# Optimization experiments

Hardware: AMD Instinct MI355X
Metric: run time of the kernel (lower is better)

## Reference

```python
import jax, jax.numpy as jnp
import numpy as np
import math

EMBED = 512
DIM2 = 768

def setup_inputs() -> dict:
    key = jax.random.key(0)
    ks = jax.random.split(key, 14)
    B, L1, L2 = 16, 2048, 1024
    s1 = 1.0 / math.sqrt(EMBED)
    s2 = 1.0 / math.sqrt(DIM2)
    inp = {
        'input_tensor1': jax.random.normal(ks[0], (B, EMBED, L1), jnp.float32),
        'input_tensor2': jax.random.normal(ks[1], (B, DIM2, L2), jnp.float32),
        # Linear params for modality 1 (512 -> 512)
        'Wq1': jax.random.normal(ks[2], (EMBED, EMBED), jnp.float32) * s1,
        'bq1': jnp.zeros((EMBED,), jnp.float32),
        'Wk1': jax.random.normal(ks[3], (EMBED, EMBED), jnp.float32) * s1,
        'bk1': jnp.zeros((EMBED,), jnp.float32),
        'Wv1': jax.random.normal(ks[4], (EMBED, EMBED), jnp.float32) * s1,
        'bv1': jnp.zeros((EMBED,), jnp.float32),
        # Linear params for modality 2 (768 -> 512)
        'Wq2': jax.random.normal(ks[5], (DIM2, EMBED), jnp.float32) * s2,
        'bq2': jnp.zeros((EMBED,), jnp.float32),
        'Wk2': jax.random.normal(ks[6], (DIM2, EMBED), jnp.float32) * s2,
        'bk2': jnp.zeros((EMBED,), jnp.float32),
        'Wv2': jax.random.normal(ks[7], (DIM2, EMBED), jnp.float32) * s2,
        'bv2': jnp.zeros((EMBED,), jnp.float32),
    }
    return inp


def reference(input_tensor1, input_tensor2,
              Wq1, bq1, Wk1, bk1, Wv1, bv1,
              Wq2, bq2, Wk2, bk2, Wv2, bv2):
    scale = 1.0 / math.sqrt(EMBED)
    # [B, C, L] -> [B, L, C]
    x1 = jnp.swapaxes(input_tensor1, 1, 2)  # [B, L1, 512]
    x2 = jnp.swapaxes(input_tensor2, 1, 2)  # [B, L2, 768]
    q1 = x1 @ Wq1 + bq1  # [B, L1, E]
    k1 = x1 @ Wk1 + bk1
    v1 = x1 @ Wv1 + bv1
    q2 = x2 @ Wq2 + bq2  # [B, L2, E]
    k2 = x2 @ Wk2 + bk2
    v2 = x2 @ Wv2 + bv2
    # direction 1: queries from modality 2 attend to modality 1
    scores1 = jnp.einsum('bif,bjf->bij', q2, k1) * scale  # [B, L2, L1]
    probs1 = jax.nn.sigmoid(scores1)
    ctx1 = jnp.einsum('bij,bjf->bif', probs1, v1)  # [B, L2, E]
    # direction 2: queries from modality 1 attend to modality 2
    scores2 = jnp.einsum('bif,bjf->bij', q1, k2) * scale  # [B, L1, L2]
    probs2 = jax.nn.sigmoid(scores2)
    ctx2 = jnp.einsum('bij,bjf->bif', probs2, v2)  # [B, L1, E]
    return (ctx2, probs2, ctx1, probs1)
```

## Files before the change

kernel.cpp:

```cpp
#include <hip/hip_runtime.h>
#include <hip/hip_bf16.h>

#define DEVFN __device__ __forceinline__

typedef __attribute__((ext_vector_type(4))) float f32x4;
typedef __attribute__((ext_vector_type(8))) short s16x8;
typedef __attribute__((ext_vector_type(2))) short s16x2;
typedef __attribute__((ext_vector_type(8))) __bf16 bf16x8;

union FragU { s16x8 s; bf16x8 b; };

DEVFN short f2bs(float x) {
  union { __hip_bfloat16 h; short s; } u;
  u.h = __float2bfloat16(x);
  return u.s;
}

DEVFN void gload16(const void* g, void* l) {
  __builtin_amdgcn_global_load_lds(
      (const __attribute__((address_space(1))) void*)g,
      (__attribute__((address_space(3))) void*)l, 16, 0, 0);
}

__global__ __launch_bounds__(256) void transpose_cvt(
    const float* __restrict__ in, short* __restrict__ out, int C, int L) {
  __shared__ float tile[64][33];
  const int l0 = blockIdx.x * 32, c0 = blockIdx.y * 64;
  const size_t base = (size_t)blockIdx.z * C * L;
  const int tx = threadIdx.x, ty = threadIdx.y;
#pragma unroll
  for (int i = ty; i < 64; i += 8)
    tile[i][tx] = in[base + (size_t)(c0 + i) * L + l0 + tx];
  __syncthreads();
#pragma unroll
  for (int i = ty; i < 32; i += 8) {
    s16x2 v;
    v[0] = f2bs(tile[2 * tx][i]);
    v[1] = f2bs(tile[2 * tx + 1][i]);
    *(s16x2*)&out[base + (size_t)(l0 + i) * C + c0 + 2 * tx] = v;
  }
}

__global__ __launch_bounds__(256) void prep_weights(
    const float* __restrict__ Wq1, const float* __restrict__ Wk1,
    const float* __restrict__ Wv1, const float* __restrict__ Wq2,
    const float* __restrict__ Wk2, const float* __restrict__ Wv2,
    short* wq1t, short* wk1t, short* wv1t,
    short* wq2t, short* wk2t, short* wv2t,
    const float* __restrict__ bq1, const float* __restrict__ bk1,
    const float* __restrict__ bq2, const float* __restrict__ bk2,
    float* b1c, float* b2c) {
  const int z = blockIdx.z;
  if (z == 6) {
    if (blockIdx.y != 0 || blockIdx.x >= 8) return;
    const int bx = blockIdx.x;
    const int tid = threadIdx.y * 32 + threadIdx.x;
    const int i = (bx & 3) * 256 + tid;
    const float* s = (bx < 4) ? ((i < 512) ? bq1 : bk1)
                              : ((i < 512) ? bq2 : bk2);
    float* d = (bx < 4) ? b1c : b2c;
    d[i] = s[i & 511];
    return;
  }
  const float* W; short* O; int C;
  switch (z) {
    case 0: W = Wq1; O = wq1t; C = 512; break;
    case 1: W = Wk1; O = wk1t; C = 512; break;
    case 2: W = Wv1; O = wv1t; C = 512; break;
    case 3: W = Wq2; O = wq2t; C = 768; break;
    case 4: W = Wk2; O = wk2t; C = 768; break;
    default: W = Wv2; O = wv2t; C = 768; break;
  }
  if (blockIdx.y * 64 >= (unsigned)C) return;
  const int L = 512;
  __shared__ float tile[64][33];
  const int l0 = blockIdx.x * 32, c0 = blockIdx.y * 64;
  const int tx = threadIdx.x, ty = threadIdx.y;
#pragma unroll
  for (int i = ty; i < 64; i += 8)
    tile[i][tx] = W[(size_t)(c0 + i) * L + l0 + tx];
  __syncthreads();
#pragma unroll
  for (int i = ty; i < 32; i += 8) {
    s16x2 v;
    v[0] = f2bs(tile[2 * tx][i]);
    v[1] = f2bs(tile[2 * tx + 1][i]);
    *(s16x2*)&O[(size_t)(l0 + i) * C + c0 + 2 * tx] = v;
  }
}

template <int OUTMODE, int BIASMODE>
__global__ __launch_bounds__(512, 2) void gemm8(
    const short* __restrict__ Ap, const short* __restrict__ Btp,
    const float* __restrict__ bias, void* __restrict__ Cptr,
    short* __restrict__ C2p,
    int K, int lda, int ldb, int ldc,
    long long sA, long long sB, long long sC, float scale) {
  __shared__ __align__(16) char smem[4 * 32768];
  const int tid = threadIdx.x;
  const int lane = tid & 63, wid = tid >> 6;
  const int wm = wid >> 2, wn = wid & 3;
  const int zb = blockIdx.z;
  const int m0 = blockIdx.y * 256, n0 = blockIdx.x * 256;
  const char* Ab = (const char*)(Ap + (size_t)zb * sA);
  const char* Bb = (const char*)(Btp + (size_t)zb * sB);
  const size_t lda2 = (size_t)lda * 2, ldb2 = (size_t)ldb * 2;

  int s_r[2], s_cb[2];
#pragma unroll
  for (int i = 0; i < 2; ++i) {
    const int d = i * 8192 + tid * 16;
    const int line = d >> 7, half = (d >> 6) & 1, q = d & 63;
    s_r[i] = line * 2 + half;
    s_cb[i] = q ^ ((line & 3) << 4);
  }

  f32x4 acc[8][4] = {};
  const int frow = lane & 15, fkg = lane >> 4;

  int ra[8], rb[4];
#pragma unroll
  for (int mf = 0; mf < 8; ++mf) {
    const int R = wm * 128 + mf * 16 + frow;
    ra[mf] = (R >> 1) * 128 + (R & 1) * 64 + ((fkg * 16) ^ (((R >> 1) & 3) << 4));
  }
#pragma unroll
  for (int nf = 0; nf < 4; ++nf) {
    const int R = wn * 64 + nf * 16 + frow;
    rb[nf] = (R >> 1) * 128 + (R & 1) * 64 + ((fkg * 16) ^ (((R >> 1) & 3) << 4));
  }

  const int NT = K >> 5;

#define STAGE8(t)                                                        \
  {                                                                      \
    char* base_ = smem + ((t) & 3) * 32768;                              \
    const size_t kb_ = (size_t)(t) * 64;                                 \
    _Pragma("unroll")                                                    \
    for (int i = 0; i < 2; ++i) {                                        \
      gload16(Ab + (size_t)(m0 + s_r[i]) * lda2 + kb_ + s_cb[i],         \
              base_ + i * 8192 + tid * 16);                              \
      gload16(Bb + (size_t)(n0 + s_r[i]) * ldb2 + kb_ + s_cb[i],         \
              base_ + 16384 + i * 8192 + tid * 16);                      \
    }                                                                    \
  }

  STAGE8(0);
  if (NT > 1) STAGE8(1);
  if (NT > 2) STAGE8(2);
  if (NT > 2)      asm volatile("s_waitcnt vmcnt(8)" ::: "memory");
  else if (NT > 1) asm volatile("s_waitcnt vmcnt(4)" ::: "memory");
  else             asm volatile("s_waitcnt vmcnt(0)" ::: "memory");
  __builtin_amdgcn_sched_barrier(0);
  __builtin_amdgcn_s_barrier();
  __builtin_amdgcn_sched_barrier(0);

  for (int t = 0; t < NT; ++t) {
    if (t + 3 < NT) STAGE8(t + 3);
    const char* la = smem + (t & 3) * 32768;
    const char* lb = la + 16384;
    FragU fa[8], fb[4];
#pragma unroll
    for (int mf = 0; mf < 8; ++mf) fa[mf].s = *(const s16x8*)(la + ra[mf]);
#pragma unroll
    for (int nf = 0; nf < 4; ++nf) fb[nf].s = *(const s16x8*)(lb + rb[nf]);
    __builtin_amdgcn_s_setprio(1);
#pragma unroll
    for (int mf = 0; mf < 8; ++mf)
#pragma unroll
      for (int nf = 0; nf < 4; ++nf)
        acc[mf][nf] = __builtin_amdgcn_mfma_f32_16x16x32_bf16(
            fa[mf].b, fb[nf].b, acc[mf][nf], 0, 0, 0);
    __builtin_amdgcn_s_setprio(0);
    if (t + 3 < NT) {
      asm volatile("s_waitcnt vmcnt(8)" ::: "memory");
    } else if (t + 2 < NT) {
      asm volatile("s_waitcnt vmcnt(4)" ::: "memory");
    } else if (t + 1 < NT) {
      asm volatile("s_waitcnt vmcnt(0)" ::: "memory");
    } else {
      break;
    }
    __builtin_amdgcn_sched_barrier(0);
    __builtin_amdgcn_s_barrier();
    __builtin_amdgcn_sched_barrier(0);
  }
#undef STAGE8

  const int rbase = (lane >> 4) * 4, cbase = lane & 15;
#pragma unroll
  for (int mf = 0; mf < 8; ++mf) {
#pragma unroll
    for (int nf = 0; nf < 4; ++nf) {
      const int gcol = n0 + wn * 64 + nf * 16 + cbase;
      float bn = (BIASMODE == 1) ? bias[gcol] : 0.f;
#pragma unroll
      for (int r = 0; r < 4; ++r) {
        const int grow = m0 + wm * 128 + mf * 16 + rbase + r;
        const size_t idx = (size_t)zb * sC + (size_t)grow * ldc + gcol;
        float v = acc[mf][nf][r];
        if constexpr (BIASMODE == 2) v += bias[grow]; else v += bn;
        if constexpr (OUTMODE == 0) {
          ((short*)Cptr)[idx] = f2bs(v);
        } else if constexpr (OUTMODE == 1) {
          ((float*)Cptr)[idx] = v;
        } else if constexpr (OUTMODE == 2) {
          ((float*)Cptr)[idx] = 1.0f / (1.0f + __expf(-v * scale));
        } else {
          float p = 1.0f / (1.0f + __expf(-v * scale));
          ((float*)Cptr)[idx] = p;
          C2p[idx] = f2bs(p);
        }
      }
    }
  }
}

template <int OUTMODE, int BIASMODE, int AF32>
__global__ __launch_bounds__(256) void gemm_bt(
    const void* __restrict__ Aptr, const short* __restrict__ Btp,
    const float* __restrict__ bias, void* __restrict__ Cptr,
    short* __restrict__ C2p,
    int K, int lda, int ldb, int ldc,
    long long sA, long long sB, long long sC, float scale) {
  __shared__ __align__(16) short lsA[128 * 64];
  __shared__ __align__(16) short lsB[128 * 64];
  const int tid = threadIdx.x;
  const int lane = tid & 63, wid = tid >> 6;
  const int zb = blockIdx.z;
  const int m0 = blockIdx.y * 128, n0 = blockIdx.x * 128;
  const short* Ab = AF32 ? nullptr : (const short*)Aptr + (size_t)zb * sA;
  const float* Af = AF32 ? (const float*)Aptr + (size_t)zb * sA : nullptr;
  const short* Bt = Btp + (size_t)zb * sB;

  f32x4 acc[4][4] = {};
  const int woffM = (wid >> 1) * 64, woffN = (wid & 1) * 64;
  const int frow = lane & 15, fkg = lane >> 4;

  for (int k0 = 0; k0 < K; k0 += 64) {
    if (k0) __syncthreads();
    if constexpr (!AF32) {
#pragma unroll
      for (int i = 0; i < 4; ++i) {
        const int f = i * 4096 + tid * 16;
        const int row = f >> 7, colb = f & 127;
        gload16((const char*)Ab + ((size_t)(m0 + row) * lda + k0) * 2 + colb,
                (char*)lsA + f);
      }
    } else {
#pragma unroll
      for (int i = 0; i < 8; ++i) {
        int f = tid + i * 256;
        int row = f >> 4, c4 = f & 15;
        f32x4 v = *(const f32x4*)&Af[(size_t)(m0 + row) * lda + k0 + c4 * 4];
        union { short s[4]; unsigned long long q; } cv;
#pragma unroll
        for (int j = 0; j < 4; ++j) cv.s[j] = f2bs(v[j]);
        *(unsigned long long*)&lsA[row * 64 + c4 * 4] = cv.q;
      }
    }
#pragma unroll
    for (int i = 0; i < 4; ++i) {
      const int f = i * 4096 + tid * 16;
      const int row = f >> 7, colb = f & 127;
      gload16((const char*)Bt + ((size_t)(n0 + row) * ldb + k0) * 2 + colb,
              (char*)lsB + f);
    }
    __syncthreads();
#pragma unroll
    for (int kk = 0; kk < 2; ++kk) {
      const int kb = kk * 32 + fkg * 8;
      FragU fa[4], fb[4];
#pragma unroll
      for (int mf = 0; mf < 4; ++mf)
        fa[mf].s = *(const s16x8*)&lsA[(woffM + mf * 16 + frow) * 64 + kb];
#pragma unroll
      for (int nf = 0; nf < 4; ++nf)
        fb[nf].s = *(const s16x8*)&lsB[(woffN + nf * 16 + frow) * 64 + kb];
#pragma unroll
      for (int mf = 0; mf < 4; ++mf)
#pragma unroll
        for (int nf = 0; nf < 4; ++nf)
          acc[mf][nf] = __builtin_amdgcn_mfma_f32_16x16x32_bf16(
              fa[mf].b, fb[nf].b, acc[mf][nf], 0, 0, 0);
    }
  }

  const int rbase = (lane >> 4) * 4, cbase = lane & 15;
#pragma unroll
  for (int mf = 0; mf < 4; ++mf) {
#pragma unroll
    for (int nf = 0; nf < 4; ++nf) {
      const int gcol = n0 + woffN + nf * 16 + cbase;
      float bn = (BIASMODE == 1) ? bias[gcol] : 0.f;
#pragma unroll
      for (int r = 0; r < 4; ++r) {
        const int grow = m0 + woffM + mf * 16 + rbase + r;
        const size_t idx = (size_t)zb * sC + (size_t)grow * ldc + gcol;
        float v = acc[mf][nf][r];
        if constexpr (BIASMODE == 2) v += bias[grow]; else v += bn;
        if constexpr (OUTMODE == 0) {
          ((short*)Cptr)[idx] = f2bs(v);
        } else if constexpr (OUTMODE == 1) {
          ((float*)Cptr)[idx] = v;
        } else if constexpr (OUTMODE == 2) {
          ((float*)Cptr)[idx] = 1.0f / (1.0f + __expf(-v * scale));
        } else {
          float p = 1.0f / (1.0f + __expf(-v * scale));
          ((float*)Cptr)[idx] = p;
          C2p[idx] = f2bs(p);
        }
      }
    }
  }
}

extern "C" void kernel_launch(void* const* d_in, const int* in_sizes, int n_in,
                              void* d_out, int out_size, void* d_ws, size_t ws_size,
                              hipStream_t stream) {
  const float* in1 = (const float*)d_in[0];
  const float* in2 = (const float*)d_in[1];
  const float* Wq1 = (const float*)d_in[2];  const float* bq1 = (const float*)d_in[3];
  const float* Wk1 = (const float*)d_in[4];  const float* bk1 = (const float*)d_in[5];
  const float* Wv1 = (const float*)d_in[6];  const float* bv1 = (const float*)d_in[7];
  const float* Wq2 = (const float*)d_in[8];  const float* bq2 = (const float*)d_in[9];
  const float* Wk2 = (const float*)d_in[10]; const float* bk2 = (const float*)d_in[11];
  const float* Wv2 = (const float*)d_in[12]; const float* bv2 = (const float*)d_in[13];

  float* out = (float*)d_out;
  float* ctx2   = out;
  float* probs2 = out + (size_t)16 * 2048 * 512;
  float* ctx1   = probs2 + (size_t)16 * 2048 * 1024;
  float* probs1 = ctx1 + (size_t)16 * 1024 * 512;

  char* ws = (char*)d_ws;
  constexpr size_t O_WQ1T = 0;
  constexpr size_t O_WK1T = O_WQ1T + (size_t)512 * 512 * 2;
  constexpr size_t O_WV1T = O_WK1T + (size_t)512 * 512 * 2;
  constexpr size_t O_WQ2T = O_WV1T + (size_t)512 * 512 * 2;
  constexpr size_t O_WK2T = O_WQ2T + (size_t)768 * 512 * 2;
  constexpr size_t O_WV2T = O_WK2T + (size_t)768 * 512 * 2;
  constexpr size_t O_B1   = O_WV2T + (size_t)768 * 512 * 2;
  constexpr size_t O_B2   = O_B1 + 4096;
  constexpr size_t O_QK1  = O_B2 + 4096;
  constexpr size_t O_V1T  = O_QK1 + (size_t)32768 * 1024 * 2;
  constexpr size_t O_QK2  = O_V1T + (size_t)16 * 512 * 2048 * 2;
  constexpr size_t O_V2T  = O_QK2 + (size_t)16384 * 1024 * 2;
  constexpr size_t O_X1B  = O_V2T + (size_t)16 * 512 * 1024 * 2;
  constexpr size_t O_X2B  = O_X1B + (size_t)32768 * 512 * 2;
  constexpr size_t O_PB1  = O_X2B + (size_t)16384 * 768 * 2;
  constexpr size_t O_PB2  = O_PB1 + (size_t)16 * 1024 * 2048 * 2;
  constexpr size_t NEED_A = O_PB2 + (size_t)16 * 2048 * 1024 * 2;
  constexpr size_t NEED_B = O_PB1;

  short* wq1t = (short*)(ws + O_WQ1T);
  short* wk1t = (short*)(ws + O_WK1T);
  short* wv1t = (short*)(ws + O_WV1T);
  short* wq2t = (short*)(ws + O_WQ2T);
  short* wk2t = (short*)(ws + O_WK2T);
  short* wv2t = (short*)(ws + O_WV2T);
  float* b1c  = (float*)(ws + O_B1);
  float* b2c  = (float*)(ws + O_B2);
  short* qk1  = (short*)(ws + O_QK1);
  short* v1t  = (short*)(ws + O_V1T);
  short* qk2  = (short*)(ws + O_QK2);
  short* v2t  = (short*)(ws + O_V2T);
  short* x1b  = (short*)(ws + O_X1B);
  short* x2b  = (short*)(ws + O_X2B);
  short* pb1  = (short*)(ws + O_PB1);
  short* pb2  = (short*)(ws + O_PB2);

  const bool tierA = ws_size >= NEED_A;
  const bool tierB = ws_size >= NEED_B;
  if (!tierB) { x1b = (short*)probs1; x2b = (short*)probs2; }

  dim3 blk256(256), blk512(512);
  dim3 blkT(32, 8);

  transpose_cvt<<<dim3(64, 8, 16), blkT, 0, stream>>>(in1, x1b, 512, 2048);
  transpose_cvt<<<dim3(32, 12, 16), blkT, 0, stream>>>(in2, x2b, 768, 1024);
  prep_weights<<<dim3(16, 12, 7), blkT, 0, stream>>>(
      Wq1, Wk1, Wv1, Wq2, Wk2, Wv2, wq1t, wk1t, wv1t, wq2t, wk2t, wv2t,
      bq1, bk1, bq2, bk2, b1c, b2c);

  const float scale = 0.04419417382415922f;
  const short* q1p = qk1;
  const short* k1p = qk1 + 512;
  const short* q2p = qk2;
  const short* k2p = qk2 + 512;

  if (tierA) {
    gemm8<0, 1><<<dim3(4, 128, 1), blk512, 0, stream>>>(
        x1b, wq1t, b1c, qk1, nullptr, 512, 512, 512, 1024, 0, 0, 0, 1.f);
    gemm8<0, 1><<<dim3(4, 64, 1), blk512, 0, stream>>>(
        x2b, wq2t, b2c, qk2, nullptr, 768, 768, 768, 1024, 0, 0, 0, 1.f);
    gemm8<0, 2><<<dim3(8, 2, 16), blk512, 0, stream>>>(
        wv1t, x1b, bv1, v1t, nullptr, 512, 512, 512, 2048,
        0, (long long)2048 * 512, (long long)512 * 2048, 1.f);
    gemm8<0, 2><<<dim3(4, 2, 16), blk512, 0, stream>>>(
        wv2t, x2b, bv2, v2t, nullptr, 768, 768, 768, 1024,
        0, (long long)1024 * 768, (long long)512 * 1024, 1.f);
    gemm8<3, 0><<<dim3(8, 4, 16), blk512, 0, stream>>>(
        q2p, k1p, nullptr, probs1, pb1, 512, 1024, 1024, 2048,
        (long long)1024 * 1024, (long long)2048 * 1024, (long long)1024 * 2048, scale);
    gemm8<3, 0><<<dim3(4, 8, 16), blk512, 0, stream>>>(
        q1p, k2p, nullptr, probs2, pb2, 512, 1024, 1024, 1024,
        (long long)2048 * 1024, (long long)1024 * 1024, (long long)2048 * 1024, scale);
    gemm8<1, 0><<<dim3(2, 4, 16), blk512, 0, stream>>>(
        pb1, v1t, nullptr, ctx1, nullptr, 2048, 2048, 2048, 512,
        (long long)1024 * 2048, (long long)512 * 2048, (long long)1024 * 512, 1.f);
    gemm8<1, 0><<<dim3(2, 8, 16), blk512, 0, stream>>>(
        pb2, v2t, nullptr, ctx2, nullptr, 1024, 1024, 1024, 512,
        (long long)2048 * 1024, (long long)512 * 1024, (long long)2048 * 512, 1.f);
  } else {
    gemm_bt<0, 1, 0><<<dim3(8, 256, 1), blk256, 0, stream>>>(
        x1b, wq1t, b1c, qk1, nullptr, 512, 512, 512, 1024, 0, 0, 0, 1.f);
    gemm_bt<0, 1, 0><<<dim3(8, 128, 1), blk256, 0, stream>>>(
        x2b, wq2t, b2c, qk2, nullptr, 768, 768, 768, 1024, 0, 0, 0, 1.f);
    gemm_bt<0, 2, 0><<<dim3(16, 4, 16), blk256, 0, stream>>>(
        wv1t, x1b, bv1, v1t, nullptr, 512, 512, 512, 2048,
        0, (long long)2048 * 512, (long long)512 * 2048, 1.f);
    gemm_bt<0, 2, 0><<<dim3(8, 4, 16), blk256, 0, stream>>>(
        wv2t, x2b, bv2, v2t, nullptr, 768, 768, 768, 1024,
        0, (long long)1024 * 768, (long long)512 * 1024, 1.f);
    gemm_bt<2, 0, 0><<<dim3(16, 8, 16), blk256, 0, stream>>>(
        q2p, k1p, nullptr, probs1, nullptr, 512, 1024, 1024, 2048,
        (long long)1024 * 1024, (long long)2048 * 1024, (long long)1024 * 2048, scale);
    gemm_bt<2, 0, 0><<<dim3(8, 16, 16), blk256, 0, stream>>>(
        q1p, k2p, nullptr, probs2, nullptr, 512, 1024, 1024, 1024,
        (long long)2048 * 1024, (long long)1024 * 1024, (long long)2048 * 1024, scale);
    gemm_bt<1, 0, 1><<<dim3(4, 8, 16), blk256, 0, stream>>>(
        probs1, v1t, nullptr, ctx1, nullptr, 2048, 2048, 2048, 512,
        (long long)1024 * 2048, (long long)512 * 2048, (long long)1024 * 512, 1.f);
    gemm_bt<1, 0, 1><<<dim3(4, 16, 16), blk256, 0, stream>>>(
        probs2, v2t, nullptr, ctx2, nullptr, 1024, 1024, 1024, 512,
        (long long)2048 * 1024, (long long)512 * 1024, (long long)2048 * 512, 1.f);
  }
}
```

Baseline: 485.1 us.

## Split GEMM k-step into two half phases and add 128-row tile variant

The bf16 MFMA GEMM kernel is templated on the M fragment count so it can run with 128-row tiles (MR=4). The tile is then used for the v2 projection and the ctx1 product, which doubles their block counts so more CUs are busy. The main loop now issues the A and B global-to-LDS prefetches separately and splits the MFMA work into two halves, each with its own barrier and LDS wait. The goal is to interleave memory issue with compute. The extra barriers per k-step add synchronisation cost, and the smaller tiles get less data reuse.

```diff
diff --git a/kernel.cpp b/kernel.cpp
--- a/kernel.cpp
+++ b/kernel.cpp
@@ -20,6 +20,15 @@
   __builtin_amdgcn_global_load_lds(
       (const __attribute__((address_space(1))) void*)g,
       (__attribute__((address_space(3))) void*)l, 16, 0, 0);
+}
+
+template <int N> DEVFN void waitcnt_vm() {
+  if constexpr (N == 0) asm volatile("s_waitcnt vmcnt(0)" ::: "memory");
+  else if constexpr (N == 3) asm volatile("s_waitcnt vmcnt(3)" ::: "memory");
+  else if constexpr (N == 4) asm volatile("s_waitcnt vmcnt(4)" ::: "memory");
+  else if constexpr (N == 6) asm volatile("s_waitcnt vmcnt(6)" ::: "memory");
+  else if constexpr (N == 8) asm volatile("s_waitcnt vmcnt(8)" ::: "memory");
+  else static_assert(N == 0, "unsupported vmcnt");
 }
 
 __global__ __launch_bounds__(256) void transpose_cvt(
@@ -89,39 +98,47 @@
   }
 }
 
-template <int OUTMODE, int BIASMODE>
+template <int OUTMODE, int BIASMODE, int MR>
 __global__ __launch_bounds__(512, 2) void gemm8(
     const short* __restrict__ Ap, const short* __restrict__ Btp,
     const float* __restrict__ bias, void* __restrict__ Cptr,
     short* __restrict__ C2p,
     int K, int lda, int ldb, int ldc,
     long long sA, long long sB, long long sC, float scale) {
-  __shared__ __align__(16) char smem[4 * 32768];
+  constexpr int BM = MR * 32;
+  constexpr int BN = 256;
+  constexpr int LA = BM / 128;
+  constexpr int LB = BN / 128;
+  constexpr int LPT = LA + LB;
+  constexpr int ABYTES = BM * 64;
+  constexpr int BUFB = (BM + BN) * 64;
+  constexpr int MH = MR / 2;
+  __shared__ __align__(16) char smem[4 * BUFB];
   const int tid = threadIdx.x;
   const int lane = tid & 63, wid = tid >> 6;
   const int wm = wid >> 2, wn = wid & 3;
   const int zb = blockIdx.z;
-  const int m0 = blockIdx.y * 256, n0 = blockIdx.x * 256;
+  const int m0 = blockIdx.y * BM, n0 = blockIdx.x * BN;
   const char* Ab = (const char*)(Ap + (size_t)zb * sA);
   const char* Bb = (const char*)(Btp + (size_t)zb * sB);
   const size_t lda2 = (size_t)lda * 2, ldb2 = (size_t)ldb * 2;
 
   int s_r[2], s_cb[2];
 #pragma unroll
-  for (int i = 0; i < 2; ++i) {
-    const int d = i * 8192 + tid * 16;
-    const int line = d >> 7, half = (d >> 6) & 1, q = d & 63;
-    s_r[i] = line * 2 + half;
-    s_cb[i] = q ^ ((line & 3) << 4);
-  }
-
-  f32x4 acc[8][4] = {};
+  for (int j = 0; j < 2; ++j) {
+    const int d = j * 8192 + tid * 16;
+    const int line = d >> 7;
+    s_r[j] = line * 2 + ((d >> 6) & 1);
+    s_cb[j] = (d & 63) ^ ((line & 3) << 4);
+  }
+
+  f32x4 acc[MR][4] = {};
   const int frow = lane & 15, fkg = lane >> 4;
 
-  int ra[8], rb[4];
-#pragma unroll
-  for (int mf = 0; mf < 8; ++mf) {
-    const int R = wm * 128 + mf * 16 + frow;
+  int ra[MR], rb[4];
+#pragma unroll
+  for (int mf = 0; mf < MR; ++mf) {
+    const int R = wm * (MR * 16) + mf * 16 + frow;
     ra[mf] = (R >> 1) * 128 + (R & 1) * 64 + ((fkg * 16) ^ (((R >> 1) & 3) << 4));
   }
 #pragma unroll
@@ -132,52 +149,74 @@
 
   const int NT = K >> 5;
 
-#define STAGE8(t)                                                        \
+#define STAGE_A(t)                                                       \
   {                                                                      \
-    char* base_ = smem + ((t) & 3) * 32768;                              \
+    char* base_ = smem + ((t) & 3) * BUFB;                               \
     const size_t kb_ = (size_t)(t) * 64;                                 \
     _Pragma("unroll")                                                    \
-    for (int i = 0; i < 2; ++i) {                                        \
-      gload16(Ab + (size_t)(m0 + s_r[i]) * lda2 + kb_ + s_cb[i],         \
-              base_ + i * 8192 + tid * 16);                              \
-      gload16(Bb + (size_t)(n0 + s_r[i]) * ldb2 + kb_ + s_cb[i],         \
-              base_ + 16384 + i * 8192 + tid * 16);                      \
-    }                                                                    \
-  }
-
-  STAGE8(0);
-  if (NT > 1) STAGE8(1);
-  if (NT > 2) STAGE8(2);
-  if (NT > 2)      asm volatile("s_waitcnt vmcnt(8)" ::: "memory");
-  else if (NT > 1) asm volatile("s_waitcnt vmcnt(4)" ::: "memory");
-  else             asm volatile("s_waitcnt vmcnt(0)" ::: "memory");
+    for (int j = 0; j < LA; ++j)                                         \
+      gload16(Ab + (size_t)(m0 + s_r[j]) * lda2 + kb_ + s_cb[j],         \
+              base_ + j * 8192 + tid * 16);                              \
+  }
+#define STAGE_B(t)                                                       \
+  {                                                                      \
+    char* base_ = smem + ((t) & 3) * BUFB + ABYTES;                      \
+    const size_t kb_ = (size_t)(t) * 64;                                 \
+    _Pragma("unroll")                                                    \
+    for (int j = 0; j < LB; ++j)                                         \
+      gload16(Bb + (size_t)(n0 + s_r[j]) * ldb2 + kb_ + s_cb[j],         \
+              base_ + j * 8192 + tid * 16);                              \
+  }
+
+  STAGE_A(0); STAGE_B(0);
+  STAGE_A(1); STAGE_B(1);
+  STAGE_A(2); STAGE_B(2);
+  waitcnt_vm<2 * LPT>();
   __builtin_amdgcn_sched_barrier(0);
   __builtin_amdgcn_s_barrier();
   __builtin_amdgcn_sched_barrier(0);
 
   for (int t = 0; t < NT; ++t) {
-    if (t + 3 < NT) STAGE8(t + 3);
-    const char* la = smem + (t & 3) * 32768;
-    const char* lb = la + 16384;
-    FragU fa[8], fb[4];
-#pragma unroll
-    for (int mf = 0; mf < 8; ++mf) fa[mf].s = *(const s16x8*)(la + ra[mf]);
+    const char* la = smem + (t & 3) * BUFB;
+    const char* lb = la + ABYTES;
+    FragU fa[MR], fb[4];
+    if (t + 3 < NT) STAGE_A(t + 3);
+#pragma unroll
+    for (int mf = 0; mf < MH; ++mf) fa[mf].s = *(const s16x8*)(la + ra[mf]);
 #pragma unroll
     for (int nf = 0; nf < 4; ++nf) fb[nf].s = *(const s16x8*)(lb + rb[nf]);
+    __builtin_amdgcn_s_barrier();
+    asm volatile("s_waitcnt lgkmcnt(0)" ::: "memory");
+    __builtin_amdgcn_sched_barrier(0);
     __builtin_amdgcn_s_setprio(1);
 #pragma unroll
-    for (int mf = 0; mf < 8; ++mf)
+    for (int mf = 0; mf < MH; ++mf)
+#pragma unroll
+      for (int nf = 0; nf < 4; ++nf)
+        acc[mf][nf] = __builtin_amdgcn_mfma_f32_16x16x32_bf16(
+            fa[mf].b, fb[nf].b, acc[mf][nf], 0, 0, 0);
+    __builtin_amdgcn_s_setprio(0);
+    __builtin_amdgcn_s_barrier();
+    if (t + 3 < NT) STAGE_B(t + 3);
+#pragma unroll
+    for (int mf = MH; mf < MR; ++mf) fa[mf].s = *(const s16x8*)(la + ra[mf]);
+    __builtin_amdgcn_s_barrier();
+    asm volatile("s_waitcnt lgkmcnt(0)" ::: "memory");
+    __builtin_amdgcn_sched_barrier(0);
+    __builtin_amdgcn_s_setprio(1);
+#pragma unroll
+    for (int mf = MH; mf < MR; ++mf)
 #pragma unroll
       for (int nf = 0; nf < 4; ++nf)
         acc[mf][nf] = __builtin_amdgcn_mfma_f32_16x16x32_bf16(
             fa[mf].b, fb[nf].b, acc[mf][nf], 0, 0, 0);
     __builtin_amdgcn_s_setprio(0);
     if (t + 3 < NT) {
-      asm volatile("s_waitcnt vmcnt(8)" ::: "memory");
+      waitcnt_vm<2 * LPT>();
     } else if (t + 2 < NT) {
-      asm volatile("s_waitcnt vmcnt(4)" ::: "memory");
+      waitcnt_vm<LPT>();
     } else if (t + 1 < NT) {
-      asm volatile("s_waitcnt vmcnt(0)" ::: "memory");
+      waitcnt_vm<0>();
     } else {
       break;
     }
@@ -185,18 +224,19 @@
     __builtin_amdgcn_s_barrier();
     __builtin_amdgcn_sched_barrier(0);
   }
-#undef STAGE8
+#undef STAGE_A
+#undef STAGE_B
 
   const int rbase = (lane >> 4) * 4, cbase = lane & 15;
 #pragma unroll
-  for (int mf = 0; mf < 8; ++mf) {
+  for (int mf = 0; mf < MR; ++mf) {
 #pragma unroll
     for (int nf = 0; nf < 4; ++nf) {
       const int gcol = n0 + wn * 64 + nf * 16 + cbase;
       float bn = (BIASMODE == 1) ? bias[gcol] : 0.f;
 #pragma unroll
       for (int r = 0; r < 4; ++r) {
-        const int grow = m0 + wm * 128 + mf * 16 + rbase + r;
+        const int grow = m0 + wm * (MR * 16) + mf * 16 + rbase + r;
         const size_t idx = (size_t)zb * sC + (size_t)grow * ldc + gcol;
         float v = acc[mf][nf][r];
         if constexpr (BIASMODE == 2) v += bias[grow]; else v += bn;
@@ -390,26 +430,26 @@
   const short* k2p = qk2 + 512;
 
   if (tierA) {
-    gemm8<0, 1><<<dim3(4, 128, 1), blk512, 0, stream>>>(
+    gemm8<0, 1, 8><<<dim3(4, 128, 1), blk512, 0, stream>>>(
         x1b, wq1t, b1c, qk1, nullptr, 512, 512, 512, 1024, 0, 0, 0, 1.f);
-    gemm8<0, 1><<<dim3(4, 64, 1), blk512, 0, stream>>>(
+    gemm8<0, 1, 8><<<dim3(4, 64, 1), blk512, 0, stream>>>(
         x2b, wq2t, b2c, qk2, nullptr, 768, 768, 768, 1024, 0, 0, 0, 1.f);
-    gemm8<0, 2><<<dim3(8, 2, 16), blk512, 0, stream>>>(
+    gemm8<0, 2, 8><<<dim3(8, 2, 16), blk512, 0, stream>>>(
         wv1t, x1b, bv1, v1t, nullptr, 512, 512, 512, 2048,
         0, (long long)2048 * 512, (long long)512 * 2048, 1.f);
-    gemm8<0, 2><<<dim3(4, 2, 16), blk512, 0, stream>>>(
+    gemm8<0, 2, 4><<<dim3(4, 4, 16), blk512, 0, stream>>>(
         wv2t, x2b, bv2, v2t, nullptr, 768, 768, 768, 1024,
         0, (long long)1024 * 768, (long long)512 * 1024, 1.f);
-    gemm8<3, 0><<<dim3(8, 4, 16), blk512, 0, stream>>>(
+    gemm8<3, 0, 8><<<dim3(8, 4, 16), blk512, 0, stream>>>(
         q2p, k1p, nullptr, probs1, pb1, 512, 1024, 1024, 2048,
         (long long)1024 * 1024, (long long)2048 * 1024, (long long)1024 * 2048, scale);
-    gemm8<3, 0><<<dim3(4, 8, 16), blk512, 0, stream>>>(
+    gemm8<3, 0, 8><<<dim3(4, 8, 16), blk512, 0, stream>>>(
         q1p, k2p, nullptr, probs2, pb2, 512, 1024, 1024, 1024,
         (long long)2048 * 1024, (long long)1024 * 1024, (long long)2048 * 1024, scale);
-    gemm8<1, 0><<<dim3(2, 4, 16), blk512, 0, stream>>>(
+    gemm8<1, 0, 4><<<dim3(2, 8, 16), blk512, 0, stream>>>(
         pb1, v1t, nullptr, ctx1, nullptr, 2048, 2048, 2048, 512,
         (long long)1024 * 2048, (long long)512 * 2048, (long long)1024 * 512, 1.f);
-    gemm8<1, 0><<<dim3(2, 8, 16), blk512, 0, stream>>>(
+    gemm8<1, 0, 8><<<dim3(2, 8, 16), blk512, 0, stream>>>(
         pb2, v2t, nullptr, ctx2, nullptr, 1024, 1024, 1024, 512,
         (long long)2048 * 1024, (long long)512 * 1024, (long long)2048 * 512, 1.f);
   } else {
```

Result: faster. 468.8 us (-3.4%).
